# Performance work log

Hardware: AMD Instinct MI355X
Metric: run time of the kernel (lower is better)

Reference implementation:

```python
import jax, jax.numpy as jnp
import numpy as np

B, H, S, D = 2, 12, 2048, 64

def setup_inputs() -> dict:
    key = jax.random.key(0)
    kq, kk, kv, km = jax.random.split(key, 4)
    return {
        "q": jax.random.normal(kq, (B, H, S, D), dtype=jnp.float32),
        "k": jax.random.normal(kk, (B, H, S, D), dtype=jnp.float32),
        "v": jax.random.normal(kv, (B, H, S, D), dtype=jnp.float32),
        "mask": jax.random.normal(km, (B, 1, S, S), dtype=jnp.float32),
    }

def reference(q, k, v, mask):
    # scores: [B,H,S,S] = Q @ K^T + mask (additive, broadcast over heads)
    scores = jnp.einsum("bhqd,bhkd->bhqk", q, k) + mask
    probs = jax.nn.softmax(scores, axis=-1)
    return jnp.einsum("bhqk,bhkd->bhqd", probs, v)
```

## Files before the change

kernel.cpp:

```cpp
#include <hip/hip_runtime.h>
#include <hip/hip_bf16.h>
#include <stdint.h>

#define S_LEN 2048
#define D_DIM 64
#define HEADS 12
#define KVB   64
#define QBLK  64
#define NTILES (S_LEN / KVB)
#define BH    (2 * HEADS)
#define TILE_BYTES 8192
#define KH_OFF ((size_t)0)
#define KL_OFF ((size_t)BH * NTILES * TILE_BYTES)
#define VT_OFF ((size_t)2 * BH * NTILES * TILE_BYTES)
#define WS_NEED ((size_t)3 * BH * NTILES * TILE_BYTES)

typedef __attribute__((ext_vector_type(8))) short bf16x8;
typedef __attribute__((ext_vector_type(4))) float f32x4;

__device__ __forceinline__ unsigned short f2bf(float x) {
    union { float f; uint32_t u; } v; v.f = x;
    uint32_t r = v.u + 0x7FFFu + ((v.u >> 16) & 1u);
    return (unsigned short)(r >> 16);
}
__device__ __forceinline__ float bf2f(unsigned short h) {
    union { uint32_t u; float f; } t; t.u = ((uint32_t)h) << 16; return t.f;
}
__device__ __forceinline__ void split2(float x, unsigned short& h, unsigned short& l) {
    h = f2bf(x);
    l = f2bf(x - bf2f(h));
}
__device__ __forceinline__ void gload16(const void* g, void* l) {
    __builtin_amdgcn_global_load_lds(
        (const __attribute__((address_space(1))) void*)g,
        (__attribute__((address_space(3))) void*)l, 16, 0, 0);
}

__global__ __launch_bounds__(256, 4)
void convert_kv(const float* __restrict__ K, const float* __restrict__ V,
                unsigned char* __restrict__ ws)
{
    __shared__ unsigned char kh_s[8192];
    __shared__ unsigned char kl_s[8192];
    __shared__ unsigned char vt_s[8192];

    const int blk = blockIdx.x;
    const int bh  = blk >> 5;
    const int t   = blk & 31;
    const long qkv_base = (long)bh * S_LEN * D_DIM;
    const int tid = threadIdx.x;
    const int k0 = t * KVB;

    const float* kp = K + qkv_base + (long)k0 * D_DIM;
    #pragma unroll
    for (int it = 0; it < 4; ++it) {
        int i   = tid + 256 * it;
        int row = i >> 4;
        int c4  = i & 15;
        float4 x = *(const float4*)(kp + row * 64 + c4 * 4);
        unsigned short h0, l0, h1, l1, h2, l2, h3, l3;
        split2(x.x, h0, l0); split2(x.y, h1, l1);
        split2(x.z, h2, l2); split2(x.w, h3, l3);
        int off = row * 128 + ((c4 * 8) ^ ((row & 7) << 4));
        *(uint2*)(kh_s + off) = make_uint2(((uint32_t)h1 << 16) | h0, ((uint32_t)h3 << 16) | h2);
        *(uint2*)(kl_s + off) = make_uint2(((uint32_t)l1 << 16) | l0, ((uint32_t)l3 << 16) | l2);
    }

    const float* vp = V + qkv_base + (long)k0 * D_DIM;
    int d = tid & 63, a = tid >> 6;
    #pragma unroll
    for (int h = 0; h < 2; ++h) {
        int kk0 = 32 * h + 8 * a;
        float e0 = vp[(kk0 + 0) * 64 + d], e1 = vp[(kk0 + 1) * 64 + d];
        float e2 = vp[(kk0 + 2) * 64 + d], e3 = vp[(kk0 + 3) * 64 + d];
        float e4 = vp[(kk0 + 4) * 64 + d], e5 = vp[(kk0 + 5) * 64 + d];
        float e6 = vp[(kk0 + 6) * 64 + d], e7 = vp[(kk0 + 7) * 64 + d];
        uint32_t w0 = ((uint32_t)f2bf(e1) << 16) | f2bf(e0);
        uint32_t w1 = ((uint32_t)f2bf(e3) << 16) | f2bf(e2);
        uint32_t w2 = ((uint32_t)f2bf(e5) << 16) | f2bf(e4);
        uint32_t w3 = ((uint32_t)f2bf(e7) << 16) | f2bf(e6);
        int off = d * 128 + ((kk0 * 2) ^ ((d & 7) << 4));
        *(uint4*)(vt_s + off) = make_uint4(w0, w1, w2, w3);
    }
    __syncthreads();

    unsigned char* kh = ws + KH_OFF + (size_t)blk * TILE_BYTES;
    unsigned char* kl = ws + KL_OFF + (size_t)blk * TILE_BYTES;
    unsigned char* vt = ws + VT_OFF + (size_t)blk * TILE_BYTES;
    #pragma unroll
    for (int i = 0; i < 2; ++i) {
        int X = tid * 16 + i * 4096;
        *(uint4*)(kh + X) = *(const uint4*)(kh_s + X);
        *(uint4*)(kl + X) = *(const uint4*)(kl_s + X);
        *(uint4*)(vt + X) = *(const uint4*)(vt_s + X);
    }
}

__device__ __forceinline__ void stage_tiles(const unsigned char* khT, const unsigned char* klT,
                                            const unsigned char* vtT,
                                            unsigned char* kh_d, unsigned char* kl_d,
                                            unsigned char* vt_d, int wave, int lane)
{
    #pragma unroll
    for (int j = 0; j < 2; ++j) {
        int o2 = wave * 2048 + j * 1024;
        gload16(khT + o2 + lane * 16, kh_d + o2);
        gload16(klT + o2 + lane * 16, kl_d + o2);
        gload16(vtT + o2 + lane * 16, vt_d + o2);
    }
}

__global__ __launch_bounds__(256, 3)
void attn_fwd_db(const float* __restrict__ Q, const float* __restrict__ M,
                 const unsigned char* __restrict__ ws, float* __restrict__ O)
{
    __shared__ unsigned char klds_h[2][8192];
    __shared__ unsigned char klds_l[2][8192];
    __shared__ unsigned char vlds[2][8192];

    const int bid  = blockIdx.x;
    const int bh   = bid >> 5;
    const int qb   = bid & 31;
    const int b    = bh / HEADS;
    const long qkv_base  = (long)bh * S_LEN * D_DIM;
    const long mask_base = (long)b * S_LEN * S_LEN;

    const int tid  = threadIdx.x;
    const int wave = tid >> 6;
    const int lane = tid & 63;
    const int c    = lane & 15;
    const int g    = lane >> 4;
    const int sw   = (c & 7) << 4;

    const int qrow = qb * QBLK + wave * 16 + c;

    bf16x8 qfh[2], qfl[2];
    {
        const float* qp = Q + qkv_base + (long)qrow * D_DIM;
        #pragma unroll
        for (int f = 0; f < 2; ++f) {
            float4 x0 = *(const float4*)(qp + f * 32 + 8 * g);
            float4 x1 = *(const float4*)(qp + f * 32 + 8 * g + 4);
            float e[8] = { x0.x, x0.y, x0.z, x0.w, x1.x, x1.y, x1.z, x1.w };
            bf16x8 th, tl;
            #pragma unroll
            for (int j = 0; j < 8; ++j) {
                unsigned short h, l;
                split2(e[j], h, l);
                th[j] = (short)h; tl[j] = (short)l;
            }
            qfh[f] = th; qfl[f] = tl;
        }
    }

    const unsigned char* khB = ws + KH_OFF + (size_t)bh * NTILES * TILE_BYTES;
    const unsigned char* klB = ws + KL_OFF + (size_t)bh * NTILES * TILE_BYTES;
    const unsigned char* vtB = ws + VT_OFF + (size_t)bh * NTILES * TILE_BYTES;
    const float* mrow = M + mask_base + (long)qrow * S_LEN;

    f32x4 o[4] = {};
    float m_run = -INFINITY, l_run = 0.f;

    stage_tiles(khB, klB, vtB, klds_h[0], klds_l[0], vlds[0], wave, lane);
    f32x4 mreg[4], nreg[4];
    #pragma unroll
    for (int kt = 0; kt < 4; ++kt)
        mreg[kt] = *(const f32x4*)(mrow + 16 * kt + 4 * g);
    __syncthreads();

    int cur = 0;
    for (int t0 = 0; t0 < NTILES; ++t0) {
        if (t0 + 1 < NTILES) {
            stage_tiles(khB + (size_t)(t0 + 1) * TILE_BYTES,
                        klB + (size_t)(t0 + 1) * TILE_BYTES,
                        vtB + (size_t)(t0 + 1) * TILE_BYTES,
                        klds_h[cur ^ 1], klds_l[cur ^ 1], vlds[cur ^ 1], wave, lane);
            #pragma unroll
            for (int kt = 0; kt < 4; ++kt)
                nreg[kt] = *(const f32x4*)(mrow + (t0 + 1) * 64 + 16 * kt + 4 * g);
        }

        f32x4 st[4];
        #pragma unroll
        for (int kt = 0; kt < 4; ++kt) {
            const unsigned char* bh_ = klds_h[cur] + (16 * kt + c) * 128;
            const unsigned char* bl_ = klds_l[cur] + (16 * kt + c) * 128;
            bf16x8 kh0 = *(const bf16x8*)(bh_ + ((16 * g) ^ sw));
            bf16x8 kh1 = *(const bf16x8*)(bh_ + ((64 + 16 * g) ^ sw));
            bf16x8 kl0 = *(const bf16x8*)(bl_ + ((16 * g) ^ sw));
            bf16x8 kl1 = *(const bf16x8*)(bl_ + ((64 + 16 * g) ^ sw));
            f32x4 acc = {};
            acc = __builtin_amdgcn_mfma_f32_16x16x32_bf16(kh0, qfl[0], acc, 0, 0, 0);
            acc = __builtin_amdgcn_mfma_f32_16x16x32_bf16(kh1, qfl[1], acc, 0, 0, 0);
            acc = __builtin_amdgcn_mfma_f32_16x16x32_bf16(kl0, qfh[0], acc, 0, 0, 0);
            acc = __builtin_amdgcn_mfma_f32_16x16x32_bf16(kl1, qfh[1], acc, 0, 0, 0);
            acc = __builtin_amdgcn_mfma_f32_16x16x32_bf16(kh0, qfh[0], acc, 0, 0, 0);
            acc = __builtin_amdgcn_mfma_f32_16x16x32_bf16(kh1, qfh[1], acc, 0, 0, 0);
            st[kt] = acc;
        }

        float p[4][4];
        float tmax = -INFINITY;
        #pragma unroll
        for (int kt = 0; kt < 4; ++kt)
            #pragma unroll
            for (int r = 0; r < 4; ++r) {
                float sc = st[kt][r] + mreg[kt][r];
                p[kt][r] = sc;
                tmax = fmaxf(tmax, sc);
            }
        tmax = fmaxf(tmax, __shfl_xor(tmax, 16, 64));
        tmax = fmaxf(tmax, __shfl_xor(tmax, 32, 64));
        float m_new = fmaxf(m_run, tmax);
        float scale = __expf(m_run - m_new);
        float tsum = 0.f;
        #pragma unroll
        for (int kt = 0; kt < 4; ++kt)
            #pragma unroll
            for (int r = 0; r < 4; ++r) {
                float e = __expf(p[kt][r] - m_new);
                p[kt][r] = e;
                tsum += e;
            }
        tsum += __shfl_xor(tsum, 16, 64);
        tsum += __shfl_xor(tsum, 32, 64);
        l_run = l_run * scale + tsum;
        m_run = m_new;
        #pragma unroll
        for (int mt = 0; mt < 4; ++mt) o[mt] *= scale;

        uint32_t w[4][2];
        #pragma unroll
        for (int kt = 0; kt < 4; ++kt) {
            w[kt][0] = ((uint32_t)f2bf(p[kt][1]) << 16) | f2bf(p[kt][0]);
            w[kt][1] = ((uint32_t)f2bf(p[kt][3]) << 16) | f2bf(p[kt][2]);
        }
        bf16x8 pf[2];
        const bool hi_half = (lane & 32) != 0;
        #pragma unroll
        for (int f = 0; f < 2; ++f) {
            uint32_t words[4];
            #pragma unroll
            for (int pp = 0; pp < 4; ++pp) {
                int srcl = 16 * (2 * (g & 1) + (pp >> 1)) + c;
                int addr = srcl << 2;
                int lo = __builtin_amdgcn_ds_bpermute(addr, (int)w[2 * f][pp & 1]);
                int hi = __builtin_amdgcn_ds_bpermute(addr, (int)w[2 * f + 1][pp & 1]);
                words[pp] = hi_half ? (uint32_t)hi : (uint32_t)lo;
            }
            union { uint32_t u[4]; bf16x8 v; } cv;
            cv.u[0] = words[0]; cv.u[1] = words[1];
            cv.u[2] = words[2]; cv.u[3] = words[3];
            pf[f] = cv.v;
        }

        #pragma unroll
        for (int f = 0; f < 2; ++f) {
            #pragma unroll
            for (int mt = 0; mt < 4; ++mt) {
                const unsigned char* base = vlds[cur] + (16 * mt + c) * 128;
                bf16x8 vf = *(const bf16x8*)(base + ((64 * f + 16 * g) ^ sw));
                o[mt] = __builtin_amdgcn_mfma_f32_16x16x32_bf16(vf, pf[f], o[mt], 0, 0, 0);
            }
        }

        __syncthreads();
        cur ^= 1;
        #pragma unroll
        for (int kt = 0; kt < 4; ++kt) mreg[kt] = nreg[kt];
    }

    float inv = 1.0f / l_run;
    float* op = O + qkv_base + (long)qrow * D_DIM;
    #pragma unroll
    for (int mt = 0; mt < 4; ++mt) {
        float4 x = make_float4(o[mt][0] * inv, o[mt][1] * inv,
                               o[mt][2] * inv, o[mt][3] * inv);
        *(float4*)(op + 16 * mt + 4 * g) = x;
    }
}

__global__ __launch_bounds__(256, 3)
void attn_fwd(const float* __restrict__ Q, const float* __restrict__ K,
              const float* __restrict__ V, const float* __restrict__ M,
              float* __restrict__ O)
{
    __shared__ unsigned char klds_h[64 * 128];
    __shared__ unsigned char klds_l[64 * 128];
    __shared__ unsigned char vlds[64 * 128];

    const int bid  = blockIdx.x;
    const int bh   = bid >> 5;
    const int qb   = bid & 31;
    const int b    = bh / HEADS;
    const long qkv_base  = (long)bh * S_LEN * D_DIM;
    const long mask_base = (long)b * S_LEN * S_LEN;

    const int tid  = threadIdx.x;
    const int wave = tid >> 6;
    const int lane = tid & 63;
    const int c    = lane & 15;
    const int g    = lane >> 4;
    const int sw   = (c & 7) << 4;

    const int qrow = qb * QBLK + wave * 16 + c;

    bf16x8 qfh[2], qfl[2];
    {
        const float* qp = Q + qkv_base + (long)qrow * D_DIM;
        #pragma unroll
        for (int f = 0; f < 2; ++f) {
            float4 x0 = *(const float4*)(qp + f * 32 + 8 * g);
            float4 x1 = *(const float4*)(qp + f * 32 + 8 * g + 4);
            float e[8] = { x0.x, x0.y, x0.z, x0.w, x1.x, x1.y, x1.z, x1.w };
            bf16x8 th, tl;
            #pragma unroll
            for (int j = 0; j < 8; ++j) {
                unsigned short h, l;
                split2(e[j], h, l);
                th[j] = (short)h; tl[j] = (short)l;
            }
            qfh[f] = th; qfl[f] = tl;
        }
    }

    f32x4 o[4] = {};
    float m_run = -INFINITY, l_run = 0.f;
    const float* mrow = M + mask_base + (long)qrow * S_LEN;

    for (int t0 = 0; t0 < NTILES; ++t0) {
        const int k0 = t0 * KVB;
        {
            const float* kp = K + qkv_base + (long)k0 * D_DIM;
            #pragma unroll
            for (int it = 0; it < 4; ++it) {
                int i   = tid + 256 * it;
                int row = i >> 4;
                int c4  = i & 15;
                float4 x = *(const float4*)(kp + row * 64 + c4 * 4);
                unsigned short h0, l0, h1, l1, h2, l2, h3, l3;
                split2(x.x, h0, l0); split2(x.y, h1, l1);
                split2(x.z, h2, l2); split2(x.w, h3, l3);
                int off = row * 128 + ((c4 * 8) ^ ((row & 7) << 4));
                *(uint2*)(klds_h + off) =
                    make_uint2(((uint32_t)h1 << 16) | h0, ((uint32_t)h3 << 16) | h2);
                *(uint2*)(klds_l + off) =
                    make_uint2(((uint32_t)l1 << 16) | l0, ((uint32_t)l3 << 16) | l2);
            }
        }
        {
            const float* vp = V + qkv_base + (long)k0 * D_DIM;
            int d = tid & 63, a = tid >> 6;
            #pragma unroll
            for (int h = 0; h < 2; ++h) {
                int kk0 = 32 * h + 8 * a;
                float e0 = vp[(kk0 + 0) * 64 + d], e1 = vp[(kk0 + 1) * 64 + d];
                float e2 = vp[(kk0 + 2) * 64 + d], e3 = vp[(kk0 + 3) * 64 + d];
                float e4 = vp[(kk0 + 4) * 64 + d], e5 = vp[(kk0 + 5) * 64 + d];
                float e6 = vp[(kk0 + 6) * 64 + d], e7 = vp[(kk0 + 7) * 64 + d];
                uint32_t w0 = ((uint32_t)f2bf(e1) << 16) | f2bf(e0);
                uint32_t w1 = ((uint32_t)f2bf(e3) << 16) | f2bf(e2);
                uint32_t w2 = ((uint32_t)f2bf(e5) << 16) | f2bf(e4);
                uint32_t w3 = ((uint32_t)f2bf(e7) << 16) | f2bf(e6);
                int off = d * 128 + ((kk0 * 2) ^ ((d & 7) << 4));
                *(uint4*)(vlds + off) = make_uint4(w0, w1, w2, w3);
            }
        }
        __syncthreads();

        f32x4 st[4];
        #pragma unroll
        for (int kt = 0; kt < 4; ++kt) {
            const unsigned char* bh_ = klds_h + (16 * kt + c) * 128;
            const unsigned char* bl_ = klds_l + (16 * kt + c) * 128;
            bf16x8 kh0 = *(const bf16x8*)(bh_ + ((16 * g) ^ sw));
            bf16x8 kh1 = *(const bf16x8*)(bh_ + ((64 + 16 * g) ^ sw));
            bf16x8 kl0 = *(const bf16x8*)(bl_ + ((16 * g) ^ sw));
            bf16x8 kl1 = *(const bf16x8*)(bl_ + ((64 + 16 * g) ^ sw));
            f32x4 acc = {};
            acc = __builtin_amdgcn_mfma_f32_16x16x32_bf16(kh0, qfl[0], acc, 0, 0, 0);
            acc = __builtin_amdgcn_mfma_f32_16x16x32_bf16(kh1, qfl[1], acc, 0, 0, 0);
            acc = __builtin_amdgcn_mfma_f32_16x16x32_bf16(kl0, qfh[0], acc, 0, 0, 0);
            acc = __builtin_amdgcn_mfma_f32_16x16x32_bf16(kl1, qfh[1], acc, 0, 0, 0);
            acc = __builtin_amdgcn_mfma_f32_16x16x32_bf16(kh0, qfh[0], acc, 0, 0, 0);
            acc = __builtin_amdgcn_mfma_f32_16x16x32_bf16(kh1, qfh[1], acc, 0, 0, 0);
            st[kt] = acc;
        }

        float p[4][4];
        float tmax = -INFINITY;
        #pragma unroll
        for (int kt = 0; kt < 4; ++kt)
            #pragma unroll
            for (int r = 0; r < 4; ++r) {
                float sc = st[kt][r] + mrow[k0 + 16 * kt + 4 * g + r];
                p[kt][r] = sc;
                tmax = fmaxf(tmax, sc);
            }
        tmax = fmaxf(tmax, __shfl_xor(tmax, 16, 64));
        tmax = fmaxf(tmax, __shfl_xor(tmax, 32, 64));
        float m_new = fmaxf(m_run, tmax);
        float scale = __expf(m_run - m_new);
        float tsum = 0.f;
        #pragma unroll
        for (int kt = 0; kt < 4; ++kt)
            #pragma unroll
            for (int r = 0; r < 4; ++r) {
                float e = __expf(p[kt][r] - m_new);
                p[kt][r] = e;
                tsum += e;
            }
        tsum += __shfl_xor(tsum, 16, 64);
        tsum += __shfl_xor(tsum, 32, 64);
        l_run = l_run * scale + tsum;
        m_run = m_new;
        #pragma unroll
        for (int mt = 0; mt < 4; ++mt) o[mt] *= scale;

        uint32_t w[4][2];
        #pragma unroll
        for (int kt = 0; kt < 4; ++kt) {
            w[kt][0] = ((uint32_t)f2bf(p[kt][1]) << 16) | f2bf(p[kt][0]);
            w[kt][1] = ((uint32_t)f2bf(p[kt][3]) << 16) | f2bf(p[kt][2]);
        }
        bf16x8 pf[2];
        const bool hi_half = (lane & 32) != 0;
        #pragma unroll
        for (int f = 0; f < 2; ++f) {
            uint32_t words[4];
            #pragma unroll
            for (int pp = 0; pp < 4; ++pp) {
                int srcl = 16 * (2 * (g & 1) + (pp >> 1)) + c;
                int addr = srcl << 2;
                int lo = __builtin_amdgcn_ds_bpermute(addr, (int)w[2 * f][pp & 1]);
                int hi = __builtin_amdgcn_ds_bpermute(addr, (int)w[2 * f + 1][pp & 1]);
                words[pp] = hi_half ? (uint32_t)hi : (uint32_t)lo;
            }
            union { uint32_t u[4]; bf16x8 v; } cv;
            cv.u[0] = words[0]; cv.u[1] = words[1];
            cv.u[2] = words[2]; cv.u[3] = words[3];
            pf[f] = cv.v;
        }

        #pragma unroll
        for (int f = 0; f < 2; ++f) {
            #pragma unroll
            for (int mt = 0; mt < 4; ++mt) {
                const unsigned char* base = vlds + (16 * mt + c) * 128;
                bf16x8 vf = *(const bf16x8*)(base + ((64 * f + 16 * g) ^ sw));
                o[mt] = __builtin_amdgcn_mfma_f32_16x16x32_bf16(vf, pf[f], o[mt], 0, 0, 0);
            }
        }
        __syncthreads();
    }

    float inv = 1.0f / l_run;
    float* op = O + qkv_base + (long)qrow * D_DIM;
    #pragma unroll
    for (int mt = 0; mt < 4; ++mt) {
        float4 x = make_float4(o[mt][0] * inv, o[mt][1] * inv,
                               o[mt][2] * inv, o[mt][3] * inv);
        *(float4*)(op + 16 * mt + 4 * g) = x;
    }
}

extern "C" void kernel_launch(void* const* d_in, const int* in_sizes, int n_in,
                              void* d_out, int out_size, void* d_ws, size_t ws_size,
                              hipStream_t stream) {
    const float* q = (const float*)d_in[0];
    const float* k = (const float*)d_in[1];
    const float* v = (const float*)d_in[2];
    const float* m = (const float*)d_in[3];
    float* o = (float*)d_out;
    dim3 grid(BH * (S_LEN / QBLK));
    dim3 block(256);
    if (ws_size >= WS_NEED) {
        convert_kv<<<grid, block, 0, stream>>>(k, v, (unsigned char*)d_ws);
        attn_fwd_db<<<grid, block, 0, stream>>>(q, m, (const unsigned char*)d_ws, o);
    } else {
        attn_fwd<<<grid, block, 0, stream>>>(q, k, v, m, o);
    }
}
```

Before: 200.7 us.

## Split KV sequence into two halves per query block and combine partials

Adds a split-KV variant where each query block is processed by two workgroups, each covering half the key/value tiles, writing partial outputs and running max/sum to workspace. A separate combine kernel merges the halves with log-sum-exp rescaling. The 768 original blocks on a large-CU GPU underfill the machine, so doubling the grid is meant to raise occupancy and balance. The cost is an extra kernel launch and workspace round-trip, and the split kernel drops the double-buffered LDS staging, so loads are no longer overlapped with compute.

```diff
diff --git a/kernel.cpp b/kernel.cpp
--- a/kernel.cpp
+++ b/kernel.cpp
@@ -8,12 +8,18 @@
 #define KVB   64
 #define QBLK  64
 #define NTILES (S_LEN / KVB)
+#define NTILES_H (NTILES / 2)
 #define BH    (2 * HEADS)
 #define TILE_BYTES 8192
 #define KH_OFF ((size_t)0)
 #define KL_OFF ((size_t)BH * NTILES * TILE_BYTES)
 #define VT_OFF ((size_t)2 * BH * NTILES * TILE_BYTES)
 #define WS_NEED ((size_t)3 * BH * NTILES * TILE_BYTES)
+#define PARTO_OFF  WS_NEED
+#define PARTO_SIZE ((size_t)1536 * 4096 * 4)
+#define PARTML_OFF (PARTO_OFF + PARTO_SIZE)
+#define PARTML_SIZE ((size_t)1536 * 128 * 4)
+#define WS_SPLIT   (PARTML_OFF + PARTML_SIZE)
 
 typedef __attribute__((ext_vector_type(8))) short bf16x8;
 typedef __attribute__((ext_vector_type(4))) float f32x4;
@@ -107,6 +113,204 @@
         gload16(khT + o2 + lane * 16, kh_d + o2);
         gload16(klT + o2 + lane * 16, kl_d + o2);
         gload16(vtT + o2 + lane * 16, vt_d + o2);
+    }
+}
+
+__global__ __launch_bounds__(256, 6)
+void attn_split(const float* __restrict__ Q, const float* __restrict__ M,
+                const unsigned char* __restrict__ ws, float* __restrict__ ws_f)
+{
+    __shared__ unsigned char klds_h[8192];
+    __shared__ unsigned char klds_l[8192];
+    __shared__ unsigned char vlds[8192];
+
+    const int bid  = blockIdx.x;
+    const int bh   = bid >> 6;
+    const int qb   = (bid >> 1) & 31;
+    const int half = bid & 1;
+    const int b    = bh / HEADS;
+    const long qkv_base  = (long)bh * S_LEN * D_DIM;
+    const long mask_base = (long)b * S_LEN * S_LEN;
+
+    const int tid  = threadIdx.x;
+    const int wave = tid >> 6;
+    const int lane = tid & 63;
+    const int c    = lane & 15;
+    const int g    = lane >> 4;
+    const int sw   = (c & 7) << 4;
+
+    const int qrow = qb * QBLK + wave * 16 + c;
+
+    bf16x8 qfh[2], qfl[2];
+    {
+        const float* qp = Q + qkv_base + (long)qrow * D_DIM;
+        #pragma unroll
+        for (int f = 0; f < 2; ++f) {
+            float4 x0 = *(const float4*)(qp + f * 32 + 8 * g);
+            float4 x1 = *(const float4*)(qp + f * 32 + 8 * g + 4);
+            float e[8] = { x0.x, x0.y, x0.z, x0.w, x1.x, x1.y, x1.z, x1.w };
+            bf16x8 th, tl;
+            #pragma unroll
+            for (int j = 0; j < 8; ++j) {
+                unsigned short h, l;
+                split2(e[j], h, l);
+                th[j] = (short)h; tl[j] = (short)l;
+            }
+            qfh[f] = th; qfl[f] = tl;
+        }
+    }
+
+    const unsigned char* khB = ws + KH_OFF + (size_t)bh * NTILES * TILE_BYTES;
+    const unsigned char* klB = ws + KL_OFF + (size_t)bh * NTILES * TILE_BYTES;
+    const unsigned char* vtB = ws + VT_OFF + (size_t)bh * NTILES * TILE_BYTES;
+    const float* mrow = M + mask_base + (long)qrow * S_LEN;
+
+    f32x4 o[4] = {};
+    float m_run = -INFINITY, l_run = 0.f;
+
+    for (int t = 0; t < NTILES_H; ++t) {
+        const int tg = half * NTILES_H + t;
+        stage_tiles(khB + (size_t)tg * TILE_BYTES,
+                    klB + (size_t)tg * TILE_BYTES,
+                    vtB + (size_t)tg * TILE_BYTES,
+                    klds_h, klds_l, vlds, wave, lane);
+        __syncthreads();
+
+        f32x4 mreg[4];
+        #pragma unroll
+        for (int kt = 0; kt < 4; ++kt)
+            mreg[kt] = *(const f32x4*)(mrow + tg * 64 + 16 * kt + 4 * g);
+
+        f32x4 st[4];
+        #pragma unroll
+        for (int kt = 0; kt < 4; ++kt) {
+            const unsigned char* bh_ = klds_h + (16 * kt + c) * 128;
+            const unsigned char* bl_ = klds_l + (16 * kt + c) * 128;
+            bf16x8 kh0 = *(const bf16x8*)(bh_ + ((16 * g) ^ sw));
+            bf16x8 kh1 = *(const bf16x8*)(bh_ + ((64 + 16 * g) ^ sw));
+            bf16x8 kl0 = *(const bf16x8*)(bl_ + ((16 * g) ^ sw));
+            bf16x8 kl1 = *(const bf16x8*)(bl_ + ((64 + 16 * g) ^ sw));
+            f32x4 acc = {};
+            acc = __builtin_amdgcn_mfma_f32_16x16x32_bf16(kh0, qfl[0], acc, 0, 0, 0);
+            acc = __builtin_amdgcn_mfma_f32_16x16x32_bf16(kh1, qfl[1], acc, 0, 0, 0);
+            acc = __builtin_amdgcn_mfma_f32_16x16x32_bf16(kl0, qfh[0], acc, 0, 0, 0);
+            acc = __builtin_amdgcn_mfma_f32_16x16x32_bf16(kl1, qfh[1], acc, 0, 0, 0);
+            acc = __builtin_amdgcn_mfma_f32_16x16x32_bf16(kh0, qfh[0], acc, 0, 0, 0);
+            acc = __builtin_amdgcn_mfma_f32_16x16x32_bf16(kh1, qfh[1], acc, 0, 0, 0);
+            st[kt] = acc;
+        }
+
+        float p[4][4];
+        float tmax = -INFINITY;
+        #pragma unroll
+        for (int kt = 0; kt < 4; ++kt)
+            #pragma unroll
+            for (int r = 0; r < 4; ++r) {
+                float sc = st[kt][r] + mreg[kt][r];
+                p[kt][r] = sc;
+                tmax = fmaxf(tmax, sc);
+            }
+        tmax = fmaxf(tmax, __shfl_xor(tmax, 16, 64));
+        tmax = fmaxf(tmax, __shfl_xor(tmax, 32, 64));
+        float m_new = fmaxf(m_run, tmax);
+        float scale = __expf(m_run - m_new);
+        float tsum = 0.f;
+        #pragma unroll
+        for (int kt = 0; kt < 4; ++kt)
+            #pragma unroll
+            for (int r = 0; r < 4; ++r) {
+                float e = __expf(p[kt][r] - m_new);
+                p[kt][r] = e;
+                tsum += e;
+            }
+        tsum += __shfl_xor(tsum, 16, 64);
+        tsum += __shfl_xor(tsum, 32, 64);
+        l_run = l_run * scale + tsum;
+        m_run = m_new;
+        #pragma unroll
+        for (int mt = 0; mt < 4; ++mt) o[mt] *= scale;
+
+        uint32_t w[4][2];
+        #pragma unroll
+        for (int kt = 0; kt < 4; ++kt) {
+            w[kt][0] = ((uint32_t)f2bf(p[kt][1]) << 16) | f2bf(p[kt][0]);
+            w[kt][1] = ((uint32_t)f2bf(p[kt][3]) << 16) | f2bf(p[kt][2]);
+        }
+        bf16x8 pf[2];
+        const bool hi_half = (lane & 32) != 0;
+        #pragma unroll
+        for (int f = 0; f < 2; ++f) {
+            uint32_t words[4];
+            #pragma unroll
+            for (int pp = 0; pp < 4; ++pp) {
+                int srcl = 16 * (2 * (g & 1) + (pp >> 1)) + c;
+                int addr = srcl << 2;
+                int lo = __builtin_amdgcn_ds_bpermute(addr, (int)w[2 * f][pp & 1]);
+                int hi = __builtin_amdgcn_ds_bpermute(addr, (int)w[2 * f + 1][pp & 1]);
+                words[pp] = hi_half ? (uint32_t)hi : (uint32_t)lo;
+            }
+            union { uint32_t u[4]; bf16x8 v; } cv;
+            cv.u[0] = words[0]; cv.u[1] = words[1];
+            cv.u[2] = words[2]; cv.u[3] = words[3];
+            pf[f] = cv.v;
+        }
+
+        #pragma unroll
+        for (int f = 0; f < 2; ++f) {
+            #pragma unroll
+            for (int mt = 0; mt < 4; ++mt) {
+                const unsigned char* base = vlds + (16 * mt + c) * 128;
+                bf16x8 vf = *(const bf16x8*)(base + ((64 * f + 16 * g) ^ sw));
+                o[mt] = __builtin_amdgcn_mfma_f32_16x16x32_bf16(vf, pf[f], o[mt], 0, 0, 0);
+            }
+        }
+        __syncthreads();
+    }
+
+    float* po = ws_f + PARTO_OFF / 4 + (size_t)bid * 4096;
+    #pragma unroll
+    for (int mt = 0; mt < 4; ++mt) {
+        float4 x = make_float4(o[mt][0], o[mt][1], o[mt][2], o[mt][3]);
+        *(float4*)(po + (wave * 16 + c) * 64 + 16 * mt + 4 * g) = x;
+    }
+    float* pml = ws_f + PARTML_OFF / 4 + (size_t)bid * 128;
+    if (g == 0) {
+        pml[wave * 16 + c]      = m_run;
+        pml[64 + wave * 16 + c] = l_run;
+    }
+}
+
+__global__ __launch_bounds__(256, 8)
+void combine_halves(const float* __restrict__ ws_f, float* __restrict__ O)
+{
+    const int bid2 = blockIdx.x;
+    const int bh   = bid2 >> 5;
+    const int qb   = bid2 & 31;
+    const int tid  = threadIdx.x;
+    const int row  = tid >> 2;
+    const int col  = (tid & 3) * 16;
+
+    const float* po0 = ws_f + PARTO_OFF / 4 + ((size_t)bid2 * 2 + 0) * 4096;
+    const float* po1 = ws_f + PARTO_OFF / 4 + ((size_t)bid2 * 2 + 1) * 4096;
+    const float* ml0 = ws_f + PARTML_OFF / 4 + ((size_t)bid2 * 2 + 0) * 128;
+    const float* ml1 = ws_f + PARTML_OFF / 4 + ((size_t)bid2 * 2 + 1) * 128;
+
+    float m0 = ml0[row], l0 = ml0[64 + row];
+    float m1 = ml1[row], l1 = ml1[64 + row];
+    float mx = fmaxf(m0, m1);
+    float f0 = __expf(m0 - mx), f1 = __expf(m1 - mx);
+    float inv = 1.0f / (l0 * f0 + l1 * f1);
+
+    float* op = O + ((long)bh * S_LEN + qb * QBLK + row) * D_DIM + col;
+    #pragma unroll
+    for (int j = 0; j < 4; ++j) {
+        float4 a = *(const float4*)(po0 + row * 64 + col + 4 * j);
+        float4 bq = *(const float4*)(po1 + row * 64 + col + 4 * j);
+        float4 r = make_float4((a.x * f0 + bq.x * f1) * inv,
+                               (a.y * f0 + bq.y * f1) * inv,
+                               (a.z * f0 + bq.z * f1) * inv,
+                               (a.w * f0 + bq.w * f1) * inv);
+        *(float4*)(op + 4 * j) = r;
     }
 }
 
@@ -472,12 +676,16 @@
     const float* v = (const float*)d_in[2];
     const float* m = (const float*)d_in[3];
     float* o = (float*)d_out;
-    dim3 grid(BH * (S_LEN / QBLK));
     dim3 block(256);
-    if (ws_size >= WS_NEED) {
-        convert_kv<<<grid, block, 0, stream>>>(k, v, (unsigned char*)d_ws);
-        attn_fwd_db<<<grid, block, 0, stream>>>(q, m, (const unsigned char*)d_ws, o);
+    if (ws_size >= WS_SPLIT) {
+        convert_kv<<<dim3(BH * NTILES), block, 0, stream>>>(k, v, (unsigned char*)d_ws);
+        attn_split<<<dim3(BH * 32 * 2), block, 0, stream>>>(q, m, (const unsigned char*)d_ws,
+                                                            (float*)d_ws);
+        combine_halves<<<dim3(BH * 32), block, 0, stream>>>((const float*)d_ws, o);
+    } else if (ws_size >= WS_NEED) {
+        convert_kv<<<dim3(BH * NTILES), block, 0, stream>>>(k, v, (unsigned char*)d_ws);
+        attn_fwd_db<<<dim3(BH * 32), block, 0, stream>>>(q, m, (const unsigned char*)d_ws, o);
     } else {
-        attn_fwd<<<grid, block, 0, stream>>>(q, k, v, m, o);
-    }
-}
+        attn_fwd<<<dim3(BH * 32), block, 0, stream>>>(q, k, v, m, o);
+    }
+}
```

Result: slower. 304.0 us (+51.5%).
